# Optimization experiments

Measured on AMD Instinct MI355X. Metric: run time of the kernel, lower is better.

Reference implementation:

```python
import jax, jax.numpy as jnp
import numpy as np

EPS = 1e-5

def batchnorm(x, g, b):
    # training-mode BN: batch statistics over (N,H,W), biased variance (matches torch)
    m = x.mean((0, 2, 3), keepdims=True)
    v = ((x - m) ** 2).mean((0, 2, 3), keepdims=True)
    return g[None, :, None, None] * (x - m) * jax.lax.rsqrt(v + EPS) + b[None, :, None, None]


def deform_conv2d(x, offset, mask, weight, bias):
    # torchvision deform_conv2d v2 semantics, stride=1, pad=1, dilation=1, 1 group, 1 offset group
    B, C, H, W = x.shape
    K = 9  # 3x3 kernel
    off = offset.reshape(B, K, 2, H, W)  # interleaved (dy, dx) per kernel tap
    dy, dx = off[:, :, 0], off[:, :, 1]  # [B,K,H,W]
    kr = jnp.arange(3, dtype=x.dtype) - 1.0
    k_y = jnp.repeat(kr, 3)  # [9] kernel row offsets
    k_x = jnp.tile(kr, 3)    # [9] kernel col offsets
    hh = jnp.arange(H, dtype=x.dtype)
    ww = jnp.arange(W, dtype=x.dtype)
    ph = dy + k_y[None, :, None, None] + hh[None, None, :, None]  # [B,K,H,W] sample rows
    pw = dx + k_x[None, :, None, None] + ww[None, None, None, :]  # [B,K,H,W] sample cols
    h0 = jnp.floor(ph); w0 = jnp.floor(pw)
    lh = ph - h0; lw = pw - w0
    h0i = h0.astype(jnp.int32); w0i = w0.astype(jnp.int32)

    def gather(xb, hb, wb):  # xb [C,H,W], hb/wb [K,H,W] -> [C,K,H,W]
        return xb[:, hb, wb]

    def corner(hi, wi, wgt):
        valid = (hi >= 0) & (hi < H) & (wi >= 0) & (wi < W)
        hic = jnp.clip(hi, 0, H - 1); wic = jnp.clip(wi, 0, W - 1)
        v = jax.vmap(gather)(x, hic, wic)  # [B,C,K,H,W]
        return v * (wgt * valid.astype(x.dtype))[:, None]

    samp = (corner(h0i, w0i, (1 - lh) * (1 - lw))
            + corner(h0i, w0i + 1, (1 - lh) * lw)
            + corner(h0i + 1, w0i, lh * (1 - lw))
            + corner(h0i + 1, w0i + 1, lh * lw))  # [B,C,K,H,W]
    samp = samp * mask[:, None]  # modulated (v2) mask [B,1,K,H,W]
    out = jnp.einsum('bckhw,ock->bohw', samp, weight.reshape(weight.shape[0], C, K))
    return out + bias[None, :, None, None]


def reference(x, conv1_w, bn1_g, bn1_b, off_w, off_b, dcn_w, dcn_b, norm_g, norm_b):
    flip = x[..., ::-1]
    xp = batchnorm(jnp.einsum('bchw,oc->bohw', x, conv1_w), bn1_g, bn1_b)  # 1x1 conv + BN, no relu
    concat = jnp.concatenate([flip, xp], axis=1)  # [B,2C,H,W]
    out = jax.lax.conv_general_dilated(concat, off_w, (1, 1), 'SAME',
                                       dimension_numbers=('NCHW', 'OIHW', 'NCHW'))
    out = out + off_b[None, :, None, None]  # [B,27,H,W]
    o1, o2, mask = jnp.split(out, 3, axis=1)
    offset = jnp.concatenate([o1, o2], axis=1)  # [B,18,H,W]
    mask = jax.nn.sigmoid(mask)  # [B,9,H,W]
    d = deform_conv2d(xp, offset, mask, dcn_w, dcn_b)
    return jax.nn.relu(batchnorm(d, norm_g, norm_b) + xp)


def setup_inputs() -> dict:
    key = jax.random.key(0)
    ks = jax.random.split(key, 6)
    B, C, H, W = 8, 256, 45, 80
    stdv = 1.0 / np.sqrt(C * 9)
    return {
        'x': jax.random.normal(ks[0], (B, C, H, W), jnp.float32),
        'conv1_w': jax.random.normal(ks[1], (C, C), jnp.float32) * 0.05,
        'bn1_g': jnp.ones((C,), jnp.float32),
        'bn1_b': jnp.zeros((C,), jnp.float32),
        'off_w': jax.random.normal(ks[2], (27, 2 * C, 3, 3), jnp.float32) * 0.01,
        'off_b': jax.random.normal(ks[3], (27,), jnp.float32) * 0.01,
        'dcn_w': jax.random.uniform(ks[4], (C, C, 3, 3), jnp.float32, -stdv, stdv),
        'dcn_b': jax.random.normal(ks[5], (C,), jnp.float32) * 0.01,
        'norm_g': jnp.ones((C,), jnp.float32),
        'norm_b': jnp.zeros((C,), jnp.float32),
    }
```

## Files before the change

kernel.cpp:

```cpp
#include <hip/hip_runtime.h>
#include <math.h>

#define BATCH 8
#define CH 256
#define HH 45
#define WW 80
#define HW 3600
#define PTOT 28800

typedef unsigned short u16;
typedef unsigned int   u32;
typedef __attribute__((ext_vector_type(8))) short bf16x8;
typedef __attribute__((ext_vector_type(4))) float f32x4;

struct __align__(8) us4 { u16 x, y, z, w; };

__device__ __forceinline__ u16 bf16_rne(float x) {
  u32 u = __float_as_uint(x);
  u += 0x7FFF + ((u >> 16) & 1);
  return (u16)(u >> 16);
}
__device__ __forceinline__ float bf16_f(u16 v) {
  return __uint_as_float((u32)v << 16);
}

__global__ __launch_bounds__(256) void flip_prep(
    const float* __restrict__ x, u16* __restrict__ concat,
    const float* __restrict__ conv1_w, const float* __restrict__ off_w,
    const float* __restrict__ dcn_w,
    u16* __restrict__ w1b, u16* __restrict__ wt_offb, u16* __restrict__ wt_b)
{
  __shared__ float tile[32][36];
  const int b  = blockIdx.z;
  const int c0 = blockIdx.y * 32;
  const int p0 = blockIdx.x * 32;
  int rem = HW - p0; if (rem > 32) rem = 32;
  const int t = threadIdx.x;

  {
    int linid = blockIdx.x + 113 * (blockIdx.y + 8 * blockIdx.z);
    if (linid < 2304) {
      int i = linid * 256 + t;
      if (i < 256 * 256) {
        w1b[i] = bf16_rne(conv1_w[i]);
      }
      if (i < 9 * 32 * 512) {
        int tap = i >> 14;
        int r   = i & 16383;
        int oc  = r >> 9;
        int c   = r & 511;
        float v = (oc < 27) ? off_w[((size_t)oc * 512 + c) * 9 + tap] : 0.f;
        wt_offb[i] = bf16_rne(v);
      }
      if (i < 9 * 256 * 256) {
        int c = i & 255;
        int oc = (i >> 8) & 255;
        int tap = i >> 16;
        wt_b[i] = bf16_rne(dcn_w[((size_t)oc * 256 + c) * 9 + tap]);
      }
    }
  }

  {
    int c = t >> 3, p4 = (t & 7) * 4;
    if (p4 < rem) {
      float4 v = *(const float4*)(x + ((size_t)b * CH + c0 + c) * HW + p0 + p4);
      *(float4*)&tile[c][p4] = v;
    }
  }
  __syncthreads();
  {
    int r = t >> 3, cq = (t & 7) * 4;
    if (r < rem) {
      int p = p0 + r;
      int h = p / WW, w = p - h * WW;
      int pf = h * WW + (WW - 1 - w);
      us4 o;
      o.x = bf16_rne(tile[cq + 0][r]);
      o.y = bf16_rne(tile[cq + 1][r]);
      o.z = bf16_rne(tile[cq + 2][r]);
      o.w = bf16_rne(tile[cq + 3][r]);
      *(us4*)(concat + ((size_t)b * HW + pf) * 512 + c0 + cq) = o;
    }
  }
}

__global__ __launch_bounds__(256) void conv1_mfma(
    const u16* __restrict__ concat, const u16* __restrict__ w1b,
    u16* __restrict__ out1b, float* __restrict__ part_c1)
{
  const int t = threadIdx.x;
  const int wv = t >> 6, lane = t & 63;
  const int lr = lane & 15, lk = lane >> 4;
  const int id = blockIdx.x;
  const int b  = id & 7;
  const int pt = id >> 3;
  const int oc0 = blockIdx.y * 128 + (wv & 1) * 64;
  const int p0  = pt * 128 + (wv >> 1) * 64;

  const u16* bptr[4];
#pragma unroll
  for (int nt = 0; nt < 4; nt++) {
    int pl = p0 + nt * 16 + lr;
    int pc = pl < HW ? pl : HW - 1;
    int h = pc / WW, w = pc - h * WW;
    int pf = b * HW + h * WW + (WW - 1 - w);
    bptr[nt] = concat + (size_t)pf * 512 + lk * 8;
  }
  const u16* aptr = w1b + ((size_t)(oc0 + lr)) * 256 + lk * 8;

  f32x4 acc[4][4];
#pragma unroll
  for (int mt = 0; mt < 4; mt++)
#pragma unroll
    for (int nt = 0; nt < 4; nt++) acc[mt][nt] = (f32x4)0.f;

#pragma unroll
  for (int cc = 0; cc < 8; cc++) {
    bf16x8 af[4], bfv[4];
#pragma unroll
    for (int mt = 0; mt < 4; mt++)
      af[mt] = *(const bf16x8*)(aptr + (size_t)mt * 16 * 256 + cc * 32);
#pragma unroll
    for (int nt = 0; nt < 4; nt++)
      bfv[nt] = *(const bf16x8*)(bptr[nt] + cc * 32);
#pragma unroll
    for (int mt = 0; mt < 4; mt++)
#pragma unroll
      for (int nt = 0; nt < 4; nt++)
        acc[mt][nt] = __builtin_amdgcn_mfma_f32_16x16x32_bf16(
            af[mt], bfv[nt], acc[mt][nt], 0, 0, 0);
  }

#pragma unroll
  for (int mt = 0; mt < 4; mt++) {
    int oc = oc0 + mt * 16 + lk * 4;
#pragma unroll
    for (int nt = 0; nt < 4; nt++) {
      int pl = p0 + nt * 16 + lr;
      if (pl < HW) {
        u16* dst = out1b + ((size_t)(b * CH + oc)) * HW + pl;
#pragma unroll
        for (int r = 0; r < 4; r++)
          dst[(size_t)r * HW] = bf16_rne(acc[mt][nt][r]);
      }
    }
  }

  float sv[4][4], sq[4][4];
#pragma unroll
  for (int mt = 0; mt < 4; mt++)
#pragma unroll
    for (int r = 0; r < 4; r++) { sv[mt][r] = 0.f; sq[mt][r] = 0.f; }
#pragma unroll
  for (int mt = 0; mt < 4; mt++)
#pragma unroll
    for (int nt = 0; nt < 4; nt++) {
      int pl = p0 + nt * 16 + lr;
      if (pl < HW) {
#pragma unroll
        for (int r = 0; r < 4; r++) {
          float v = acc[mt][nt][r];
          sv[mt][r] += v; sq[mt][r] += v * v;
        }
      }
    }
#pragma unroll
  for (int m = 1; m < 16; m <<= 1) {
#pragma unroll
    for (int mt = 0; mt < 4; mt++)
#pragma unroll
      for (int r = 0; r < 4; r++) {
        sv[mt][r] += __shfl_xor(sv[mt][r], m, 64);
        sq[mt][r] += __shfl_xor(sq[mt][r], m, 64);
      }
  }
  if (lr == 0) {
    int slot = (wv >> 1) + 2 * blockIdx.x + 464 * blockIdx.y;
    float* pp = part_c1 + (size_t)slot * 128 * 2;
#pragma unroll
    for (int mt = 0; mt < 4; mt++)
#pragma unroll
      for (int r = 0; r < 4; r++) {
        int ocl = (wv & 1) * 64 + mt * 16 + lk * 4 + r;
        pp[ocl * 2]     = sv[mt][r];
        pp[ocl * 2 + 1] = sq[mt][r];
      }
  }
}

__global__ __launch_bounds__(256) void stats_fin_c1(
    const float* __restrict__ part_c1, float* __restrict__ st)
{
  const int c = blockIdx.x;
  const int y = c >> 7, ocl = c & 127;
  const int t = threadIdx.x;
  const float* base = part_c1 + (size_t)y * 464 * 256 + ocl * 2;
  float s = 0.f, s2 = 0.f;
  for (int i = t; i < 464; i += 256) {
    s  += base[(size_t)i * 256];
    s2 += base[(size_t)i * 256 + 1];
  }
  __shared__ float ls[256], ls2[256];
  ls[t] = s; ls2[t] = s2;
  __syncthreads();
  for (int off = 128; off > 0; off >>= 1) {
    if (t < off) { ls[t] += ls[t + off]; ls2[t] += ls2[t + off]; }
    __syncthreads();
  }
  if (t == 0) {
    float m = ls[0] / (float)PTOT;
    float var = ls2[0] / (float)PTOT - m * m;
    st[c] = m;
    st[CH + c] = rsqrtf(var + 1e-5f);
  }
}

__global__ __launch_bounds__(256) void stats_fin_d(
    const float* __restrict__ part_d, float* __restrict__ st)
{
  const int c = blockIdx.x;
  const int t = threadIdx.x;
  float s = 0.f, s2 = 0.f;
  for (int i = t; i < 456; i += 256) {
    s  += part_d[(size_t)i * 512 + c * 2];
    s2 += part_d[(size_t)i * 512 + c * 2 + 1];
  }
  __shared__ float ls[256], ls2[256];
  ls[t] = s; ls2[t] = s2;
  __syncthreads();
  for (int off = 128; off > 0; off >>= 1) {
    if (t < off) { ls[t] += ls[t + off]; ls2[t] += ls2[t + off]; }
    __syncthreads();
  }
  if (t == 0) {
    float m = ls[0] / (float)PTOT;
    float var = ls2[0] / (float)PTOT - m * m;
    st[c] = m;
    st[CH + c] = rsqrtf(var + 1e-5f);
  }
}

__global__ __launch_bounds__(256) void norm_transpose(
    const u16* __restrict__ out1b, const float* __restrict__ st,
    const float* __restrict__ g, const float* __restrict__ bb,
    u16* __restrict__ concat)
{
  __shared__ float tile[32][36];
  const int b  = blockIdx.z;
  const int c0 = blockIdx.y * 32;
  const int p0 = blockIdx.x * 32;
  int rem = HW - p0; if (rem > 32) rem = 32;
  const int t = threadIdx.x;

  {
    int c  = t >> 3;
    int p4 = (t & 7) * 4;
    int cg = c0 + c;
    float m  = st[cg], rs = st[CH + cg];
    float sc = g[cg] * rs;
    float sh = bb[cg] - m * sc;
    if (p4 < rem) {
      size_t base = ((size_t)b * CH + cg) * HW + p0;
      us4 v4 = *(const us4*)(out1b + base + p4);
      tile[c][p4 + 0] = bf16_f(v4.x) * sc + sh;
      tile[c][p4 + 1] = bf16_f(v4.y) * sc + sh;
      tile[c][p4 + 2] = bf16_f(v4.z) * sc + sh;
      tile[c][p4 + 3] = bf16_f(v4.w) * sc + sh;
    }
  }
  __syncthreads();
  {
    int r  = t >> 3;
    int cq = (t & 7) * 4;
    if (r < rem) {
      us4 o;
      o.x = bf16_rne(tile[cq + 0][r]);
      o.y = bf16_rne(tile[cq + 1][r]);
      o.z = bf16_rne(tile[cq + 2][r]);
      o.w = bf16_rne(tile[cq + 3][r]);
      *(us4*)(concat + ((size_t)b * HW + p0 + r) * 512 + 256 + c0 + cq) = o;
    }
  }
}

__global__ __launch_bounds__(128) void off_mfma(
    const u16* __restrict__ concat, const u16* __restrict__ wt_offb,
    float* __restrict__ offp3)
{
  const int t = threadIdx.x;
  const int g = blockIdx.y;
  const int wv = t >> 6, lane = t & 63;
  const int lr = lane & 15, lk = lane >> 4;
  const int id = blockIdx.x;
  const int b    = id & 7;
  const int tile = id >> 3;
  const int pbase = tile * 64 + wv * 32;

  int   pl[2];
  int   h[2], w[2];
  bool  pv[2];
#pragma unroll
  for (int nt = 0; nt < 2; nt++) {
    int p = pbase + nt * 16 + lr;
    pv[nt] = p < HW;
    if (!pv[nt]) p = HW - 1;
    pl[nt] = p;
    h[nt] = p / WW;
    w[nt] = p - h[nt] * WW;
  }

  f32x4 acc[2][2];
#pragma unroll
  for (int mt = 0; mt < 2; mt++)
#pragma unroll
    for (int nt = 0; nt < 2; nt++) acc[mt][nt] = (f32x4)0.f;

#pragma unroll 1
  for (int tl = 0; tl < 3; tl++) {
    int tap = g * 3 + tl;
    int dy = tap / 3 - 1, dx = tap % 3 - 1;
    const u16* bp[2];
    bool valid[2];
#pragma unroll
    for (int nt = 0; nt < 2; nt++) {
      valid[nt] = ((unsigned)(h[nt] + dy) < HH) && ((unsigned)(w[nt] + dx) < WW);
      int Ps = b * HW + (valid[nt] ? (pl[nt] + dy * WW + dx) : pl[nt]);
      bp[nt] = concat + (size_t)Ps * 512 + lk * 8;
    }
    const u16* ap = wt_offb + ((size_t)tap * 32 + lr) * 512 + lk * 8;
#pragma unroll
    for (int cc = 0; cc < 16; cc++) {
      bf16x8 bfv[2];
#pragma unroll
      for (int nt = 0; nt < 2; nt++) {
        bfv[nt] = *(const bf16x8*)(bp[nt] + cc * 32);
        if (!valid[nt]) bfv[nt] = (bf16x8)(short)0;
      }
      bf16x8 af0 = *(const bf16x8*)(ap + cc * 32);
      bf16x8 af1 = *(const bf16x8*)(ap + 16 * 512 + cc * 32);
#pragma unroll
      for (int nt = 0; nt < 2; nt++) {
        acc[0][nt] = __builtin_amdgcn_mfma_f32_16x16x32_bf16(af0, bfv[nt], acc[0][nt], 0, 0, 0);
        acc[1][nt] = __builtin_amdgcn_mfma_f32_16x16x32_bf16(af1, bfv[nt], acc[1][nt], 0, 0, 0);
      }
    }
  }

#pragma unroll
  for (int nt = 0; nt < 2; nt++) {
    if (pv[nt]) {
      int P = b * HW + pl[nt];
#pragma unroll
      for (int mt = 0; mt < 2; mt++) {
        int oc = mt * 16 + lk * 4;
#pragma unroll
        for (int r = 0; r < 4; r++)
          offp3[((size_t)g * 32 + oc + r) * PTOT + P] = acc[mt][nt][r];
      }
    }
  }
}

__global__ __launch_bounds__(512) void deform_mfma(
    const u16* __restrict__ concat,
    const float* __restrict__ offp3, const float* __restrict__ off_b,
    const u16* __restrict__ wt_b,
    u16* __restrict__ dbufb, float* __restrict__ part_d)
{
  __shared__ u16    samp[64 * 256];
  __shared__ int4   sidx[9][64];
  __shared__ float4 swq[9][64];

  const int t    = threadIdx.x;
  const int wv   = t >> 6;
  const int lane = t & 63;
  const int lr = lane & 15, lk = lane >> 4;
  const int id   = blockIdx.x;
  const int b    = id & 7;
  const int tile = id >> 3;
  const int P0   = b * HW + tile * 64;
  int lim  = HW - tile * 64;
  if (lim > 64) lim = 64;

  for (int item = t; item < 9 * 64; item += 512) {
    int tap = item >> 6, pos = item & 63;
    int off = (pos < lim) ? pos : (lim - 1);
    int pl = tile * 64 + off;
    int P  = b * HW + pl;
    int h = pl / WW, w = pl - h * WW;

    float dy = off_b[2 * tap], dx = off_b[2 * tap + 1], ml = off_b[18 + tap];
#pragma unroll
    for (int g = 0; g < 3; g++) {
      const float* basep = offp3 + (size_t)g * 32 * PTOT + P;
      dy += basep[(size_t)(2 * tap    ) * PTOT];
      dx += basep[(size_t)(2 * tap + 1) * PTOT];
      ml += basep[(size_t)(18 + tap   ) * PTOT];
    }
    float m = 1.f / (1.f + expf(-ml));
    float ph = dy + (float)(tap / 3 - 1) + (float)h;
    float pw = dx + (float)(tap % 3 - 1) + (float)w;
    float h0f = floorf(ph), w0f = floorf(pw);
    float lh = ph - h0f, lw = pw - w0f;
    int h0 = (int)h0f, w0 = (int)w0f;
    int h1 = h0 + 1, w1 = w0 + 1;
    float vh0 = (h0 >= 0 && h0 < HH) ? 1.f : 0.f;
    float vh1 = (h1 >= 0 && h1 < HH) ? 1.f : 0.f;
    float vw0 = (w0 >= 0 && w0 < WW) ? 1.f : 0.f;
    float vw1 = (w1 >= 0 && w1 < WW) ? 1.f : 0.f;
    float4 wvq;
    wvq.x = (1.f - lh) * (1.f - lw) * m * vh0 * vw0;
    wvq.y = (1.f - lh) * lw         * m * vh0 * vw1;
    wvq.z = lh * (1.f - lw)         * m * vh1 * vw0;
    wvq.w = lh * lw                 * m * vh1 * vw1;
    int hc0 = min(max(h0, 0), HH - 1), hc1 = min(max(h1, 0), HH - 1);
    int wc0 = min(max(w0, 0), WW - 1), wc1 = min(max(w1, 0), WW - 1);
    int gbase = b * HW;
    int4 iv;
    iv.x = (gbase + hc0 * WW + wc0) * 512 + 256;
    iv.y = (gbase + hc0 * WW + wc1) * 512 + 256;
    iv.z = (gbase + hc1 * WW + wc0) * 512 + 256;
    iv.w = (gbase + hc1 * WW + wc1) * 512 + 256;
    swq[tap][pos]  = wvq;
    sidx[tap][pos] = iv;
  }
  __syncthreads();

  f32x4 acc[2][4];
#pragma unroll
  for (int mt = 0; mt < 2; mt++)
#pragma unroll
    for (int nt = 0; nt < 4; nt++) acc[mt][nt] = (f32x4)0.f;

  const int c4 = lane * 4;

  for (int tap = 0; tap < 9; tap++) {
#pragma unroll 2
    for (int it = 0; it < 8; it++) {
      int pos = it * 8 + wv;
      int4  iv = sidx[tap][pos];
      float4 wq = swq[tap][pos];
      uint2 u0 = *(const uint2*)(concat + iv.x + c4);
      uint2 u1 = *(const uint2*)(concat + iv.y + c4);
      uint2 u2 = *(const uint2*)(concat + iv.z + c4);
      uint2 u3 = *(const uint2*)(concat + iv.w + c4);
      float a0, a1, a2, a3;
      a0  = wq.x * __uint_as_float(u0.x << 16);
      a1  = wq.x * __uint_as_float(u0.x & 0xFFFF0000u);
      a2  = wq.x * __uint_as_float(u0.y << 16);
      a3  = wq.x * __uint_as_float(u0.y & 0xFFFF0000u);
      a0 = fmaf(wq.y, __uint_as_float(u1.x << 16), a0);
      a1 = fmaf(wq.y, __uint_as_float(u1.x & 0xFFFF0000u), a1);
      a2 = fmaf(wq.y, __uint_as_float(u1.y << 16), a2);
      a3 = fmaf(wq.y, __uint_as_float(u1.y & 0xFFFF0000u), a3);
      a0 = fmaf(wq.z, __uint_as_float(u2.x << 16), a0);
      a1 = fmaf(wq.z, __uint_as_float(u2.x & 0xFFFF0000u), a1);
      a2 = fmaf(wq.z, __uint_as_float(u2.y << 16), a2);
      a3 = fmaf(wq.z, __uint_as_float(u2.y & 0xFFFF0000u), a3);
      a0 = fmaf(wq.w, __uint_as_float(u3.x << 16), a0);
      a1 = fmaf(wq.w, __uint_as_float(u3.x & 0xFFFF0000u), a1);
      a2 = fmaf(wq.w, __uint_as_float(u3.y << 16), a2);
      a3 = fmaf(wq.w, __uint_as_float(u3.y & 0xFFFF0000u), a3);
      uint2 r;
      r.x = (__float_as_uint(a0) >> 16) | (__float_as_uint(a1) & 0xFFFF0000u);
      r.y = (__float_as_uint(a2) >> 16) | (__float_as_uint(a3) & 0xFFFF0000u);
      u32 byte = (u32)pos * 512u + (u32)c4 * 2u;
      byte ^= (u32)(pos & 7) << 4;
      *(uint2*)((char*)samp + byte) = r;
    }
    __syncthreads();

#pragma unroll 1
    for (int cc = 0; cc < 8; cc++) {
      int c0 = cc * 32;
      bf16x8 bfr[4];
#pragma unroll
      for (int nt = 0; nt < 4; nt++) {
        int pos = nt * 16 + lr;
        u32 byte = (u32)pos * 512u + (u32)(c0 + lk * 8) * 2u;
        byte ^= (u32)(pos & 7) << 4;
        bfr[nt] = *(const bf16x8*)((const char*)samp + byte);
      }
      const u16* wp = wt_b + ((size_t)tap * 256 + wv * 32 + lr) * 256
                      + c0 + lk * 8;
      bf16x8 afr[2];
#pragma unroll
      for (int mt = 0; mt < 2; mt++)
        afr[mt] = *(const bf16x8*)(wp + (size_t)mt * 16 * 256);
#pragma unroll
      for (int mt = 0; mt < 2; mt++)
#pragma unroll
        for (int nt = 0; nt < 4; nt++)
          acc[mt][nt] = __builtin_amdgcn_mfma_f32_16x16x32_bf16(
              afr[mt], bfr[nt], acc[mt][nt], 0, 0, 0);
    }
    __syncthreads();
  }

#pragma unroll
  for (int mt = 0; mt < 2; mt++) {
    int oc = wv * 32 + mt * 16 + lk * 4;
#pragma unroll
    for (int nt = 0; nt < 4; nt++) {
      int pl = tile * 64 + nt * 16 + lr;
      if (pl < HW) {
        u16* dst = dbufb + ((size_t)(b * CH + oc)) * HW + pl;
#pragma unroll
        for (int r = 0; r < 4; r++)
          dst[(size_t)r * HW] = bf16_rne(acc[mt][nt][r]);
      }
    }
  }

  float sv[2][4], sq[2][4];
#pragma unroll
  for (int mt = 0; mt < 2; mt++)
#pragma unroll
    for (int r = 0; r < 4; r++) { sv[mt][r] = 0.f; sq[mt][r] = 0.f; }
#pragma unroll
  for (int mt = 0; mt < 2; mt++)
#pragma unroll
    for (int nt = 0; nt < 4; nt++) {
      int pl = tile * 64 + nt * 16 + lr;
      if (pl < HW) {
#pragma unroll
        for (int r = 0; r < 4; r++) {
          float v = acc[mt][nt][r];
          sv[mt][r] += v; sq[mt][r] += v * v;
        }
      }
    }
#pragma unroll
  for (int m = 1; m < 16; m <<= 1) {
#pragma unroll
    for (int mt = 0; mt < 2; mt++)
#pragma unroll
      for (int r = 0; r < 4; r++) {
        sv[mt][r] += __shfl_xor(sv[mt][r], m, 64);
        sq[mt][r] += __shfl_xor(sq[mt][r], m, 64);
      }
  }
  if (lr == 0) {
    float* pp = part_d + (size_t)blockIdx.x * 512;
#pragma unroll
    for (int mt = 0; mt < 2; mt++)
#pragma unroll
      for (int r = 0; r < 4; r++) {
        int oc = wv * 32 + mt * 16 + lk * 4 + r;
        pp[oc * 2]     = sv[mt][r];
        pp[oc * 2 + 1] = sq[mt][r];
      }
  }
}

__global__ __launch_bounds__(256) void final_nchw(
    const u16* __restrict__ dbufb, const u16* __restrict__ out1b,
    const float* __restrict__ st1, const float* __restrict__ g1,
    const float* __restrict__ b1,
    const float* __restrict__ st2, const float* __restrict__ g2,
    const float* __restrict__ b2, float* __restrict__ out)
{
  u32 i4 = blockIdx.x * 256 + threadIdx.x;
  u32 e = i4 * 4;
  int row = (int)(e / HW);
  int c = row & 255;
  float m1 = st1[c], rs1 = st1[CH + c];
  float sc1 = g1[c] * rs1;
  float sh1 = b1[c] - m1 * sc1;
  float m2 = st2[c], rs2 = st2[CH + c];
  float sc2 = g2[c] * rs2;
  float sh2 = b2[c] - m2 * sc2;
  us4 dv4 = *(const us4*)(dbufb + e);
  us4 xv4 = *(const us4*)(out1b + e);
  float4 o;
  o.x = bf16_f(dv4.x) * sc2 + sh2 + bf16_f(xv4.x) * sc1 + sh1;
  o.y = bf16_f(dv4.y) * sc2 + sh2 + bf16_f(xv4.y) * sc1 + sh1;
  o.z = bf16_f(dv4.z) * sc2 + sh2 + bf16_f(xv4.z) * sc1 + sh1;
  o.w = bf16_f(dv4.w) * sc2 + sh2 + bf16_f(xv4.w) * sc1 + sh1;
  o.x = o.x > 0.f ? o.x : 0.f;
  o.y = o.y > 0.f ? o.y : 0.f;
  o.z = o.z > 0.f ? o.z : 0.f;
  o.w = o.w > 0.f ? o.w : 0.f;
  *(float4*)(out + e) = o;
}

extern "C" void kernel_launch(void* const* d_in, const int* in_sizes, int n_in,
                              void* d_out, int out_size, void* d_ws, size_t ws_size,
                              hipStream_t stream)
{
  const float* x       = (const float*)d_in[0];
  const float* conv1_w = (const float*)d_in[1];
  const float* bn1_g   = (const float*)d_in[2];
  const float* bn1_b   = (const float*)d_in[3];
  const float* off_w   = (const float*)d_in[4];
  const float* off_b   = (const float*)d_in[5];
  const float* dcn_w   = (const float*)d_in[6];
  const float* norm_g  = (const float*)d_in[8];
  const float* norm_b  = (const float*)d_in[9];
  float* out = (float*)d_out;

  char* ws = (char*)d_ws;
  size_t o = 0;
  u16*   out1b   = (u16*)  (ws + o); o += (size_t)PTOT * CH * 2;
  u16*   concat  = (u16*)  (ws + o); o += (size_t)PTOT * 512 * 2;
  u16*   dbufb   = (u16*)  (ws + o); o += (size_t)PTOT * CH * 2;
  float* offp3   = (float*)(ws + o); o += (size_t)96 * PTOT * 4;
  u16*   wt_b    = (u16*)  (ws + o); o += (size_t)9 * 256 * 256 * 2;
  u16*   wt_offb = (u16*)  (ws + o); o += (size_t)9 * 32 * 512 * 2;
  u16*   w1b     = (u16*)  (ws + o); o += (size_t)256 * 256 * 2;
  float* st      = (float*)(ws + o); o += 512 * 4;
  float* st2     = (float*)(ws + o); o += 512 * 4;
  float* part_c1 = (float*)(ws + o); o += (size_t)928 * 128 * 2 * 4;
  float* part_d  = (float*)(ws + o); o += (size_t)456 * 512 * 4;

  flip_prep<<<dim3(113, 8, 8), 256, 0, stream>>>(x, concat, conv1_w, off_w,
                                                 dcn_w, w1b, wt_offb, wt_b);
  conv1_mfma<<<dim3(232, 2), 256, 0, stream>>>(concat, w1b, out1b, part_c1);
  stats_fin_c1<<<256, 256, 0, stream>>>(part_c1, st);
  norm_transpose<<<dim3(113, 8, 8), 256, 0, stream>>>(out1b, st, bn1_g, bn1_b, concat);
  off_mfma<<<dim3(456, 3), 128, 0, stream>>>(concat, wt_offb, offp3);
  deform_mfma<<<456, 512, 0, stream>>>(concat, offp3, off_b, wt_b, dbufb, part_d);
  stats_fin_d<<<256, 256, 0, stream>>>(part_d, st2);
  final_nchw<<<7200, 256, 0, stream>>>(dbufb, out1b, st, bn1_g, bn1_b,
                                       st2, norm_g, norm_b, out);
}
```

Baseline: 231.4 us.

## Fuse offset/mask conv into deform kernel via shared-memory partial sums

Removes the separate off_mfma launch and its global offp3 buffer by having each deform_mfma block compute the 27-channel offset/mask convolution for its own 64 pixels first. The 8 waves split into 2 pixel halves × 4 tap groups, and their partial sums go into LDS reusing the samp buffer. A sync then lets the sampling-index stage reduce the four partials. This saves a launch and a global round trip but serializes the offset GEMM inside each block, with uneven tap splits (3/2/2/2 taps) across the wave groups.

```diff
diff --git a/kernel.cpp b/kernel.cpp
--- a/kernel.cpp
+++ b/kernel.cpp
@@ -284,93 +284,17 @@
   }
 }
 
-__global__ __launch_bounds__(128) void off_mfma(
+__global__ __launch_bounds__(512) void deform_mfma(
     const u16* __restrict__ concat, const u16* __restrict__ wt_offb,
-    float* __restrict__ offp3)
-{
-  const int t = threadIdx.x;
-  const int g = blockIdx.y;
-  const int wv = t >> 6, lane = t & 63;
-  const int lr = lane & 15, lk = lane >> 4;
-  const int id = blockIdx.x;
-  const int b    = id & 7;
-  const int tile = id >> 3;
-  const int pbase = tile * 64 + wv * 32;
-
-  int   pl[2];
-  int   h[2], w[2];
-  bool  pv[2];
-#pragma unroll
-  for (int nt = 0; nt < 2; nt++) {
-    int p = pbase + nt * 16 + lr;
-    pv[nt] = p < HW;
-    if (!pv[nt]) p = HW - 1;
-    pl[nt] = p;
-    h[nt] = p / WW;
-    w[nt] = p - h[nt] * WW;
-  }
-
-  f32x4 acc[2][2];
-#pragma unroll
-  for (int mt = 0; mt < 2; mt++)
-#pragma unroll
-    for (int nt = 0; nt < 2; nt++) acc[mt][nt] = (f32x4)0.f;
-
-#pragma unroll 1
-  for (int tl = 0; tl < 3; tl++) {
-    int tap = g * 3 + tl;
-    int dy = tap / 3 - 1, dx = tap % 3 - 1;
-    const u16* bp[2];
-    bool valid[2];
-#pragma unroll
-    for (int nt = 0; nt < 2; nt++) {
-      valid[nt] = ((unsigned)(h[nt] + dy) < HH) && ((unsigned)(w[nt] + dx) < WW);
-      int Ps = b * HW + (valid[nt] ? (pl[nt] + dy * WW + dx) : pl[nt]);
-      bp[nt] = concat + (size_t)Ps * 512 + lk * 8;
-    }
-    const u16* ap = wt_offb + ((size_t)tap * 32 + lr) * 512 + lk * 8;
-#pragma unroll
-    for (int cc = 0; cc < 16; cc++) {
-      bf16x8 bfv[2];
-#pragma unroll
-      for (int nt = 0; nt < 2; nt++) {
-        bfv[nt] = *(const bf16x8*)(bp[nt] + cc * 32);
-        if (!valid[nt]) bfv[nt] = (bf16x8)(short)0;
-      }
-      bf16x8 af0 = *(const bf16x8*)(ap + cc * 32);
-      bf16x8 af1 = *(const bf16x8*)(ap + 16 * 512 + cc * 32);
-#pragma unroll
-      for (int nt = 0; nt < 2; nt++) {
-        acc[0][nt] = __builtin_amdgcn_mfma_f32_16x16x32_bf16(af0, bfv[nt], acc[0][nt], 0, 0, 0);
-        acc[1][nt] = __builtin_amdgcn_mfma_f32_16x16x32_bf16(af1, bfv[nt], acc[1][nt], 0, 0, 0);
-      }
-    }
-  }
-
-#pragma unroll
-  for (int nt = 0; nt < 2; nt++) {
-    if (pv[nt]) {
-      int P = b * HW + pl[nt];
-#pragma unroll
-      for (int mt = 0; mt < 2; mt++) {
-        int oc = mt * 16 + lk * 4;
-#pragma unroll
-        for (int r = 0; r < 4; r++)
-          offp3[((size_t)g * 32 + oc + r) * PTOT + P] = acc[mt][nt][r];
-      }
-    }
-  }
-}
-
-__global__ __launch_bounds__(512) void deform_mfma(
-    const u16* __restrict__ concat,
-    const float* __restrict__ offp3, const float* __restrict__ off_b,
+    const float* __restrict__ off_b,
     const u16* __restrict__ wt_b,
     u16* __restrict__ dbufb, float* __restrict__ part_d)
 {
   __shared__ u16    samp[64 * 256];
   __shared__ int4   sidx[9][64];
   __shared__ float4 swq[9][64];
+
+  float* offpart = (float*)samp;
 
   const int t    = threadIdx.x;
   const int wv   = t >> 6;
@@ -383,20 +307,86 @@
   int lim  = HW - tile * 64;
   if (lim > 64) lim = 64;
 
+  {
+    const int ph = wv & 1;
+    const int kg = wv >> 1;
+    const int tap_lo = (kg == 0) ? 0 : (kg == 1) ? 3 : (kg == 2) ? 5 : 7;
+    const int tap_hi = (kg == 0) ? 3 : (kg == 1) ? 5 : (kg == 2) ? 7 : 9;
+
+    int pl2[2], h2[2], w2[2];
+#pragma unroll
+    for (int nt = 0; nt < 2; nt++) {
+      int p = tile * 64 + ph * 32 + nt * 16 + lr;
+      if (p >= HW) p = HW - 1;
+      pl2[nt] = p;
+      h2[nt] = p / WW;
+      w2[nt] = p - h2[nt] * WW;
+    }
+
+    f32x4 oacc[2][2];
+#pragma unroll
+    for (int mt = 0; mt < 2; mt++)
+#pragma unroll
+      for (int nt = 0; nt < 2; nt++) oacc[mt][nt] = (f32x4)0.f;
+
+#pragma unroll 1
+    for (int tap = tap_lo; tap < tap_hi; tap++) {
+      int dy = tap / 3 - 1, dx = tap % 3 - 1;
+      const u16* bp[2];
+      bool valid[2];
+#pragma unroll
+      for (int nt = 0; nt < 2; nt++) {
+        valid[nt] = ((unsigned)(h2[nt] + dy) < HH) && ((unsigned)(w2[nt] + dx) < WW);
+        int Ps = b * HW + (valid[nt] ? (pl2[nt] + dy * WW + dx) : pl2[nt]);
+        bp[nt] = concat + (size_t)Ps * 512 + lk * 8;
+      }
+      const u16* ap = wt_offb + ((size_t)tap * 32 + lr) * 512 + lk * 8;
+#pragma unroll
+      for (int cc = 0; cc < 16; cc++) {
+        bf16x8 bfv[2];
+#pragma unroll
+        for (int nt = 0; nt < 2; nt++) {
+          bfv[nt] = *(const bf16x8*)(bp[nt] + cc * 32);
+          if (!valid[nt]) bfv[nt] = (bf16x8)(short)0;
+        }
+        bf16x8 af0 = *(const bf16x8*)(ap + cc * 32);
+        bf16x8 af1 = *(const bf16x8*)(ap + 16 * 512 + cc * 32);
+#pragma unroll
+        for (int nt = 0; nt < 2; nt++) {
+          oacc[0][nt] = __builtin_amdgcn_mfma_f32_16x16x32_bf16(af0, bfv[nt], oacc[0][nt], 0, 0, 0);
+          oacc[1][nt] = __builtin_amdgcn_mfma_f32_16x16x32_bf16(af1, bfv[nt], oacc[1][nt], 0, 0, 0);
+        }
+      }
+    }
+
+#pragma unroll
+    for (int mt = 0; mt < 2; mt++) {
+#pragma unroll
+      for (int nt = 0; nt < 2; nt++) {
+        int pos = ph * 32 + nt * 16 + lr;
+#pragma unroll
+        for (int r = 0; r < 4; r++) {
+          int oc = mt * 16 + lk * 4 + r;
+          offpart[(kg * 32 + oc) * 64 + pos] = oacc[mt][nt][r];
+        }
+      }
+    }
+  }
+  __syncthreads();
+
   for (int item = t; item < 9 * 64; item += 512) {
     int tap = item >> 6, pos = item & 63;
     int off = (pos < lim) ? pos : (lim - 1);
     int pl = tile * 64 + off;
-    int P  = b * HW + pl;
     int h = pl / WW, w = pl - h * WW;
 
     float dy = off_b[2 * tap], dx = off_b[2 * tap + 1], ml = off_b[18 + tap];
 #pragma unroll
-    for (int g = 0; g < 3; g++) {
-      const float* basep = offp3 + (size_t)g * 32 * PTOT + P;
-      dy += basep[(size_t)(2 * tap    ) * PTOT];
-      dx += basep[(size_t)(2 * tap + 1) * PTOT];
-      ml += basep[(size_t)(18 + tap   ) * PTOT];
+    for (int kg = 0; kg < 4; kg++) {
+      const float* bp = offpart + (size_t)kg * 32 * 64 + off;
+      dy += bp[(2 * tap    ) * 64];
+      dx += bp[(2 * tap + 1) * 64];
+      ml += bp[(18 + tap   ) * 64];
     }
     float m = 1.f / (1.f + expf(-ml));
     float ph = dy + (float)(tap / 3 - 1) + (float)h;
@@ -605,7 +595,6 @@
   u16*   out1b   = (u16*)  (ws + o); o += (size_t)PTOT * CH * 2;
   u16*   concat  = (u16*)  (ws + o); o += (size_t)PTOT * 512 * 2;
   u16*   dbufb   = (u16*)  (ws + o); o += (size_t)PTOT * CH * 2;
-  float* offp3   = (float*)(ws + o); o += (size_t)96 * PTOT * 4;
   u16*   wt_b    = (u16*)  (ws + o); o += (size_t)9 * 256 * 256 * 2;
   u16*   wt_offb = (u16*)  (ws + o); o += (size_t)9 * 32 * 512 * 2;
   u16*   w1b     = (u16*)  (ws + o); o += (size_t)256 * 256 * 2;
@@ -619,8 +608,7 @@
   conv1_mfma<<<dim3(232, 2), 256, 0, stream>>>(concat, w1b, out1b, part_c1);
   stats_fin_c1<<<256, 256, 0, stream>>>(part_c1, st);
   norm_transpose<<<dim3(113, 8, 8), 256, 0, stream>>>(out1b, st, bn1_g, bn1_b, concat);
-  off_mfma<<<dim3(456, 3), 128, 0, stream>>>(concat, wt_offb, offp3);
-  deform_mfma<<<456, 512, 0, stream>>>(concat, offp3, off_b, wt_b, dbufb, part_d);
+  deform_mfma<<<456, 512, 0, stream>>>(concat, wt_offb, off_b, wt_b, dbufb, part_d);
   stats_fin_d<<<256, 256, 0, stream>>>(part_d, st2);
   final_nchw<<<7200, 256, 0, stream>>>(dbufb, out1b, st, bn1_g, bn1_b,
                                        st2, norm_g, norm_b, out);
```

After: 226.9 us. About the same (-1.9%).
